# Performance work log

Measured on AMD Instinct MI355X. Metric: run time of the kernel, lower is better.

The kernel has to match this reference:

```python
import jax, jax.numpy as jnp
import numpy as np

N = 100000   # nodes
E = 1600000  # edges (avg degree 16)
D = 128      # in_dim == hidden
L = 3        # num_layers
G = 512      # graphs in batch


def setup_inputs() -> dict:
    key = jax.random.key(0)
    ks = jax.random.split(key, 14)
    s = 0.05
    return {
        "x": jax.random.normal(ks[0], (N, D), jnp.float32),
        "edge_index": jax.random.randint(ks[1], (2, E), 0, N, dtype=jnp.int32),
        "batch": jnp.sort(jax.random.randint(ks[2], (N,), 0, G, dtype=jnp.int32)),
        "W1": jax.random.normal(ks[3], (L, D, D), jnp.float32) * s,
        "b1": jax.random.normal(ks[4], (L, D), jnp.float32) * s,
        "W2": jax.random.normal(ks[5], (L, D, D), jnp.float32) * s,
        "b2": jax.random.normal(ks[6], (L, D), jnp.float32) * s,
        "gamma": jax.random.uniform(ks[7], (L, D), jnp.float32, 0.5, 1.5),
        "beta": jax.random.normal(ks[8], (L, D), jnp.float32) * s,
        "run_mean": jax.random.normal(ks[9], (L, D), jnp.float32) * s,
        "run_var": jax.random.uniform(ks[10], (L, D), jnp.float32, 0.5, 1.5),
        "eps": jnp.zeros((L,), jnp.float32),
        "lin1_W": jax.random.normal(ks[11], (D, D), jnp.float32) * s,
        "lin1_b": jax.random.normal(ks[12], (D,), jnp.float32) * s,
    }


def _bn(h, g, b, m, v):
    # BatchNorm1d in eval mode (running stats)
    return (h - m) * jax.lax.rsqrt(v + 1e-5) * g + b


def reference(x, edge_index, batch, W1, b1, W2, b2, gamma, beta,
              run_mean, run_var, eps, lin1_W, lin1_b):
    n = x.shape[0]
    src, dst = edge_index[0], edge_index[1]
    h = x
    for l in range(L):  # small fixed layer count
        # GINConv: sum-aggregate neighbor features then (1+eps)*self + agg
        agg = jax.ops.segment_sum(h[src], dst, num_segments=n)  # [N, D]
        z = (1.0 + eps[l]) * h + agg
        z = jax.nn.relu(z @ W1[l] + b1[l])
        z = jax.nn.relu(z @ W2[l] + b2[l])
        h = _bn(z, gamma[l], beta[l], run_mean[l], run_var[l])
    # global_mean_pool over graph ids
    counts = jax.ops.segment_sum(jnp.ones((n,), h.dtype), batch, num_segments=G)
    pooled = jax.ops.segment_sum(h, batch, num_segments=G)
    pooled = pooled / jnp.maximum(counts, 1.0)[:, None]  # [G, D]
    # lin1 + ReLU (dropout is identity in eval)
    return jax.nn.relu(pooled @ lin1_W + lin1_b)
```

## Files before the change

### kernel.cpp

```cpp
#include <hip/hip_runtime.h>
#include <hip/hip_bf16.h>

#define NN 100000
#define NE 1600000
#define DD 128
#define NL 3
#define NG 512
#define NBLK ((NN + 255) / 256)
#define CSRP (NE + 8 * NN)
#define NBUCK ((NN + 63) / 64)
#define BSHIFT 9
#define NBUCK2 ((NN + 511) / 512)
#define ABLKS 512
#define ECHUNK (NE / ABLKS)

#define CONV_BLKS 12501
#define PREPW_BLKS 384
#define DEG_BLKS  391
#define INIT_BLKS (CONV_BLKS + PREPW_BLKS + DEG_BLKS)

typedef __attribute__((ext_vector_type(8))) short bf16x8;
typedef __attribute__((ext_vector_type(4))) float f32x4;

__device__ __forceinline__ unsigned short f2bf(float f) {
    union { float f; unsigned int u; } x; x.f = f;
    unsigned int r = x.u + 0x7FFFu + ((x.u >> 16) & 1u);
    return (unsigned short)(r >> 16);
}
__device__ __forceinline__ float bf2f(unsigned short u) {
    union { unsigned int u; float f; } x; x.u = ((unsigned int)u) << 16;
    return x.f;
}
__device__ __forceinline__ float bflo(unsigned int v) { return bf2f((unsigned short)(v & 0xffffu)); }
__device__ __forceinline__ float bfhi(unsigned int v) { return bf2f((unsigned short)(v >> 16)); }
__device__ __forceinline__ unsigned cvtpk(float lo, float hi) {
    unsigned r;
    asm("v_cvt_pk_bf16_f32 %0, %1, %2" : "=v"(r) : "v"(lo), "v"(hi));
    return r;
}

__global__ __launch_bounds__(256) void init_all(const float* __restrict__ x,
                                                unsigned short* __restrict__ h0,
                                                unsigned short* __restrict__ h1,
                                                const float* __restrict__ W1,
                                                const float* __restrict__ W2,
                                                unsigned short* __restrict__ wbf,
                                                int* __restrict__ deg) {
    int bb = blockIdx.x;
    if (bb < CONV_BLKS) {
        long long t = (long long)bb * 256 + threadIdx.x;
        long long base = t * 4;
        if (base < (long long)NN * DD) {
            float4 v = *reinterpret_cast<const float4*>(x + base);
            ushort4 p;
            p.x = f2bf(v.x); p.y = f2bf(v.y); p.z = f2bf(v.z); p.w = f2bf(v.w);
            *reinterpret_cast<ushort4*>(h0 + base) = p;
        } else if (base < (long long)(NN + 1) * DD) {
            ushort4 z = {0, 0, 0, 0};
            *reinterpret_cast<ushort4*>(h0 + base) = z;
            *reinterpret_cast<ushort4*>(h1 + base) = z;
        }
        return;
    }
    bb -= CONV_BLKS;
    if (bb < PREPW_BLKS) {
        int idx = bb * 256 + threadIdx.x;
        int k = idx & 127;
        int n = (idx >> 7) & 127;
        int w = (idx >> 14) & 1;
        int l = idx >> 15;
        const float* src = w ? W2 : W1;
        wbf[idx] = f2bf(src[(l * DD + k) * DD + n]);
        return;
    }
    bb -= PREPW_BLKS;
    int i = bb * 256 + threadIdx.x;
    if (i < NN) deg[i] = 0;
}

__global__ __launch_bounds__(256) void hist_deg(const int* __restrict__ ei,
                                                int* __restrict__ deg) {
    unsigned int e = blockIdx.x * 256u + threadIdx.x;
    atomicAdd(&deg[ei[NE + e]], 1);
}

__global__ __launch_bounds__(256) void scan1(const int* __restrict__ deg,
                                             int* __restrict__ rp,
                                             int* __restrict__ part,
                                             int* __restrict__ bhist) {
    __shared__ int s[256];
    int tid = threadIdx.x;
    int i = blockIdx.x * 256 + tid;
    int vr = (i < NN) ? deg[i] : 0;
    int v = (vr + 7) & ~7;
    s[tid] = v;
    __syncthreads();
    for (int o = 1; o < 256; o <<= 1) {
        int t = (tid >= o) ? s[tid - o] : 0;
        __syncthreads();
        s[tid] += t;
        __syncthreads();
    }
    if (i < NN) rp[i] = s[tid] - v;
    if (tid == 255) part[blockIdx.x] = s[255];
    int bs = vr;
    #pragma unroll
    for (int o = 1; o < 64; o <<= 1) bs += __shfl_xor(bs, o);
    int bucket = blockIdx.x * 4 + (tid >> 6);
    if ((tid & 63) == 0 && bucket < NBUCK) bhist[bucket] = bs;
}

__global__ __launch_bounds__(256) void scan23(int* __restrict__ rp,
                                              const int* __restrict__ part,
                                              const int* __restrict__ deg,
                                              int* __restrict__ csr) {
    __shared__ int red[256];
    int tid = threadIdx.x;
    int bid = blockIdx.x;
    int s = 0;
    for (int i = tid; i < bid; i += 256) s += part[i];
    red[tid] = s;
    __syncthreads();
    for (int o = 128; o > 0; o >>= 1) {
        if (tid < o) red[tid] += red[tid + o];
        __syncthreads();
    }
    int base = red[0];
    int i = bid * 256 + tid;
    if (i < NN) {
        int val = rp[i] + base;
        rp[i] = val;
        int d = deg[i];
        int pd = (d + 7) & ~7;
        for (int j = val + d; j < val + pd; ++j) csr[j] = NN;
        if (i == NN - 1) rp[NN] = val + pd;
    }
}

__global__ __launch_bounds__(256) void bscan(const int* __restrict__ bhist,
                                             int* __restrict__ cboff,
                                             int* __restrict__ gpos) {
    __shared__ int s[256];
    int tid = threadIdx.x;
    int sum = 0;
    if (tid < NBUCK2) {
        #pragma unroll
        for (int j = 0; j < 8; ++j) {
            int f = tid * 8 + j;
            if (f < NBUCK) sum += bhist[f];
        }
    }
    s[tid] = sum;
    __syncthreads();
    for (int o = 1; o < 256; o <<= 1) {
        int t = (tid >= o) ? s[tid - o] : 0;
        __syncthreads();
        s[tid] += t;
        __syncthreads();
    }
    if (tid < NBUCK2) {
        cboff[tid] = s[tid] - sum;
        gpos[tid] = 0;
    }
    if (tid == 0) cboff[NBUCK2] = NE;
}

__global__ __launch_bounds__(256) void binA(const int* __restrict__ ei,
                                            const int* __restrict__ cboff,
                                            int* __restrict__ gpos,
                                            int* __restrict__ ebuf) {
    __shared__ int hist[NBUCK2];
    __shared__ int sbase[NBUCK2];
    int tid = threadIdx.x;
    int e0 = blockIdx.x * ECHUNK;
    for (int i = tid; i < NBUCK2; i += 256) hist[i] = 0;
    __syncthreads();
    for (int i = tid; i < ECHUNK; i += 256) {
        int d = ei[NE + e0 + i];
        atomicAdd(&hist[d >> BSHIFT], 1);
    }
    __syncthreads();
    for (int i = tid; i < NBUCK2; i += 256) {
        int h = hist[i];
        sbase[i] = (h > 0) ? atomicAdd(&gpos[i], h) : 0;
        hist[i] = 0;
    }
    __syncthreads();
    for (int i = tid; i < ECHUNK; i += 256) {
        int s2 = ei[e0 + i];
        int d = ei[NE + e0 + i];
        int b = d >> BSHIFT;
        int pos = atomicAdd(&hist[b], 1);
        ebuf[cboff[b] + sbase[b] + pos] = s2 | ((d & 511) << 17);
    }
}

__global__ __launch_bounds__(256) void binB(const int* __restrict__ ebuf,
                                            const int* __restrict__ cboff,
                                            const int* __restrict__ rp,
                                            int* __restrict__ csr) {
    __shared__ int lcnt[512];
    __shared__ int rpl[512];
    int b = blockIdx.x;
    int tid = threadIdx.x;
    int nb = b << BSHIFT;
    for (int i = tid; i < 512; i += 256) {
        int node = nb + i;
        rpl[i] = (node < NN) ? rp[node] : 0;
        lcnt[i] = 0;
    }
    __syncthreads();
    int st = cboff[b], en = cboff[b + 1];
    for (int i = st + tid; i < en; i += 256) {
        int v = ebuf[i];
        int s2 = v & 0x1FFFF;
        int dl = v >> 17;
        int pos = atomicAdd(&lcnt[dl], 1);
        csr[rpl[dl] + pos] = s2;
    }
}

__global__ __launch_bounds__(256) void layer_fused(
    const unsigned short* __restrict__ hin,
    const int* __restrict__ rp,
    const int* __restrict__ csr,
    const unsigned short* __restrict__ w1t,
    const unsigned short* __restrict__ w2t,
    const float* __restrict__ b1,
    const float* __restrict__ b2,
    const float* __restrict__ gamma,
    const float* __restrict__ beta,
    const float* __restrict__ rmean,
    const float* __restrict__ rvar,
    const float* __restrict__ epsv,
    unsigned short* __restrict__ hout)
{
    __shared__ unsigned short z_lds[16 * 136];
    const int tid = threadIdx.x;
    const int lane = tid & 63;
    const int wave = tid >> 6;
    const int gid = lane >> 4;
    const int lg = lane & 15;
    const int row0 = blockIdx.x * 16;
    const float epl = 1.0f + epsv[0];
    const size_t lgo = (size_t)lg * 8;

#define ACC8(v) do { \
    acc[0] += bflo((v).x); acc[1] += bfhi((v).x); \
    acc[2] += bflo((v).y); acc[3] += bfhi((v).y); \
    acc[4] += bflo((v).z); acc[5] += bfhi((v).z); \
    acc[6] += bflo((v).w); acc[7] += bfhi((v).w); } while (0)

    const int rbase = row0 + (wave << 2);
    int pv = (lane < 5) ? rp[rbase + lane] : 0;
    const int st = __shfl(pv, gid);
    const int en = __shfl(pv, gid + 1);
    const int myrow = rbase + gid;

    float acc[8];
    {
        uint4 sv = *reinterpret_cast<const uint4*>(hin + (size_t)myrow * DD + lgo);
        acc[0] = epl * bflo(sv.x); acc[1] = epl * bfhi(sv.x);
        acc[2] = epl * bflo(sv.y); acc[3] = epl * bfhi(sv.y);
        acc[4] = epl * bflo(sv.z); acc[5] = epl * bfhi(sv.z);
        acc[6] = epl * bflo(sv.w); acc[7] = epl * bfhi(sv.w);
    }
    for (int c0 = st; c0 < en; c0 += 8) {
        int4 idA = *reinterpret_cast<const int4*>(csr + c0);
        int4 idB = *reinterpret_cast<const int4*>(csr + c0 + 4);
        uint4 v0 = *reinterpret_cast<const uint4*>(hin + (size_t)idA.x * DD + lgo);
        uint4 v1 = *reinterpret_cast<const uint4*>(hin + (size_t)idA.y * DD + lgo);
        uint4 v2 = *reinterpret_cast<const uint4*>(hin + (size_t)idA.z * DD + lgo);
        uint4 v3 = *reinterpret_cast<const uint4*>(hin + (size_t)idA.w * DD + lgo);
        uint4 v4 = *reinterpret_cast<const uint4*>(hin + (size_t)idB.x * DD + lgo);
        uint4 v5 = *reinterpret_cast<const uint4*>(hin + (size_t)idB.y * DD + lgo);
        uint4 v6 = *reinterpret_cast<const uint4*>(hin + (size_t)idB.z * DD + lgo);
        uint4 v7 = *reinterpret_cast<const uint4*>(hin + (size_t)idB.w * DD + lgo);
        ACC8(v0); ACC8(v1); ACC8(v2); ACC8(v3);
        ACC8(v4); ACC8(v5); ACC8(v6); ACC8(v7);
    }
    {
        uint4 pk;
        pk.x = cvtpk(acc[0], acc[1]);
        pk.y = cvtpk(acc[2], acc[3]);
        pk.z = cvtpk(acc[4], acc[5]);
        pk.w = cvtpk(acc[6], acc[7]);
        *reinterpret_cast<uint4*>(&z_lds[((wave << 2) + gid) * 136 + lg * 8]) = pk;
    }
    __syncthreads();

    const int l15 = lane & 15;
    const int kq = lane >> 4;
    const int colbase = wave << 5;

    bf16x8 afr[4];
    #pragma unroll
    for (int kk = 0; kk < 4; ++kk)
        afr[kk] = *reinterpret_cast<const bf16x8*>(&z_lds[l15 * 136 + kk * 32 + kq * 8]);
    __syncthreads();

    f32x4 acc4[2];
    #pragma unroll
    for (int nt = 0; nt < 2; ++nt) acc4[nt] = (f32x4){0.f, 0.f, 0.f, 0.f};
    #pragma unroll
    for (int nt = 0; nt < 2; ++nt) {
        #pragma unroll
        for (int kk = 0; kk < 4; ++kk) {
            bf16x8 bfr = *reinterpret_cast<const bf16x8*>(
                w1t + (colbase + nt * 16 + l15) * DD + kk * 32 + kq * 8);
            acc4[nt] = __builtin_amdgcn_mfma_f32_16x16x32_bf16(afr[kk], bfr, acc4[nt], 0, 0, 0);
        }
    }

    #pragma unroll
    for (int nt = 0; nt < 2; ++nt) {
        int col = colbase + nt * 16 + l15;
        float bv = b1[col];
        #pragma unroll
        for (int r = 0; r < 4; ++r) {
            int zr = kq * 4 + r;
            float v = acc4[nt][r] + bv;
            v = v > 0.f ? v : 0.f;
            z_lds[zr * 136 + col] = f2bf(v);
        }
    }
    __syncthreads();

    #pragma unroll
    for (int kk = 0; kk < 4; ++kk)
        afr[kk] = *reinterpret_cast<const bf16x8*>(&z_lds[l15 * 136 + kk * 32 + kq * 8]);
    #pragma unroll
    for (int nt = 0; nt < 2; ++nt) acc4[nt] = (f32x4){0.f, 0.f, 0.f, 0.f};
    #pragma unroll
    for (int nt = 0; nt < 2; ++nt) {
        #pragma unroll
        for (int kk = 0; kk < 4; ++kk) {
            bf16x8 bfr = *reinterpret_cast<const bf16x8*>(
                w2t + (colbase + nt * 16 + l15) * DD + kk * 32 + kq * 8);
            acc4[nt] = __builtin_amdgcn_mfma_f32_16x16x32_bf16(afr[kk], bfr, acc4[nt], 0, 0, 0);
        }
    }

    #pragma unroll
    for (int nt = 0; nt < 2; ++nt) {
        int col = colbase + nt * 16 + l15;
        float bv = b2[col];
        float ga = gamma[col];
        float be = beta[col];
        float mu = rmean[col];
        float inv = rsqrtf(rvar[col] + 1e-5f);
        #pragma unroll
        for (int r = 0; r < 4; ++r) {
            int zr = kq * 4 + r;
            float v = acc4[nt][r] + bv;
            v = v > 0.f ? v : 0.f;
            v = (v - mu) * inv * ga + be;
            hout[(size_t)(row0 + zr) * DD + col] = f2bf(v);
        }
    }
#undef ACC8
}

__global__ __launch_bounds__(256) void pool_final(const unsigned short* __restrict__ h,
                                                  const int* __restrict__ batch,
                                                  const float* __restrict__ W,
                                                  const float* __restrict__ b,
                                                  float* __restrict__ out) {
    int g = blockIdx.x;
    int t = threadIdx.x;
    int c2 = t & 63;
    int qu = t >> 6;

    int lo = 0, hi = NN;
    while (lo < hi) { int mid = (lo + hi) >> 1; if (batch[mid] < g) lo = mid + 1; else hi = mid; }
    int start = lo;
    hi = NN;
    while (lo < hi) { int mid = (lo + hi) >> 1; if (batch[mid] < g + 1) lo = mid + 1; else hi = mid; }
    int end = lo;

    float ax = 0.f, ay = 0.f;
    for (int i = start + qu; i < end; i += 4) {
        unsigned u = *reinterpret_cast<const unsigned*>(h + (size_t)i * DD + c2 * 2);
        ax += bflo(u); ay += bfhi(u);
    }

    __shared__ float ps[4][DD];
    ps[qu][c2 * 2] = ax;
    ps[qu][c2 * 2 + 1] = ay;
    __syncthreads();
    if (t < DD) {
        float inv = 1.0f / fmaxf((float)(end - start), 1.0f);
        ps[0][t] = (ps[0][t] + ps[1][t] + ps[2][t] + ps[3][t]) * inv;
    }
    __syncthreads();
    if (t < DD) {
        float o = b[t];
        #pragma unroll 8
        for (int k = 0; k < DD; ++k)
            o += ps[0][k] * W[k * DD + t];
        out[(size_t)g * DD + t] = fmaxf(o, 0.f);
    }
}

extern "C" void kernel_launch(void* const* d_in, const int* in_sizes, int n_in,
                              void* d_out, int out_size, void* d_ws, size_t ws_size,
                              hipStream_t stream) {
    const float* x     = (const float*)d_in[0];
    const int*   ei    = (const int*)d_in[1];
    const int*   batch = (const int*)d_in[2];
    const float* W1    = (const float*)d_in[3];
    const float* b1    = (const float*)d_in[4];
    const float* W2    = (const float*)d_in[5];
    const float* b2    = (const float*)d_in[6];
    const float* gamma = (const float*)d_in[7];
    const float* beta  = (const float*)d_in[8];
    const float* rmean = (const float*)d_in[9];
    const float* rvar  = (const float*)d_in[10];
    const float* eps   = (const float*)d_in[11];
    const float* lin1W = (const float*)d_in[12];
    const float* lin1b = (const float*)d_in[13];
    float* out = (float*)d_out;

    char* ws = (char*)d_ws;
    size_t off = 0;
    auto alloc = [&](size_t bytes) {
        void* p = ws + off;
        off = (off + bytes + 255) & ~(size_t)255;
        return p;
    };
    unsigned short* h0  = (unsigned short*)alloc((size_t)(NN + 1) * DD * 2);
    unsigned short* h1  = (unsigned short*)alloc((size_t)(NN + 1) * DD * 2);
    int* rp    = (int*)alloc((size_t)(NN + 1) * 4);
    int* deg   = (int*)alloc((size_t)NN * 4);
    int* part  = (int*)alloc(512 * 4);
    int* bhist = (int*)alloc((size_t)NBUCK * 4);
    int* cboff = (int*)alloc((size_t)(NBUCK2 + 1) * 4);
    int* gpos  = (int*)alloc((size_t)NBUCK2 * 4);
    int* csr   = (int*)alloc((size_t)CSRP * 4);
    int* ebuf  = (int*)alloc((size_t)NE * 4);
    unsigned short* wbf = (unsigned short*)alloc((size_t)NL * 2 * DD * DD * 2);

    init_all<<<INIT_BLKS, 256, 0, stream>>>(x, h0, h1, W1, W2, wbf, deg);

    hist_deg<<<NE / 256, 256, 0, stream>>>(ei, deg);
    scan1<<<NBLK, 256, 0, stream>>>(deg, rp, part, bhist);
    scan23<<<NBLK, 256, 0, stream>>>(rp, part, deg, csr);
    bscan<<<1, 256, 0, stream>>>(bhist, cboff, gpos);
    binA<<<ABLKS, 256, 0, stream>>>(ei, cboff, gpos, ebuf);
    binB<<<NBUCK2, 256, 0, stream>>>(ebuf, cboff, rp, csr);

    const int lgrid = NN / 16;
    layer_fused<<<lgrid, 256, 0, stream>>>(
        h0, rp, csr, wbf + 0 * DD * DD, wbf + 1 * DD * DD,
        b1 + 0 * DD, b2 + 0 * DD, gamma + 0 * DD, beta + 0 * DD,
        rmean + 0 * DD, rvar + 0 * DD, eps + 0, h1);
    layer_fused<<<lgrid, 256, 0, stream>>>(
        h1, rp, csr, wbf + 2 * DD * DD, wbf + 3 * DD * DD,
        b1 + 1 * DD, b2 + 1 * DD, gamma + 1 * DD, beta + 1 * DD,
        rmean + 1 * DD, rvar + 1 * DD, eps + 1, h0);
    layer_fused<<<lgrid, 256, 0, stream>>>(
        h0, rp, csr, wbf + 4 * DD * DD, wbf + 5 * DD * DD,
        b1 + 2 * DD, b2 + 2 * DD, gamma + 2 * DD, beta + 2 * DD,
        rmean + 2 * DD, rvar + 2 * DD, eps + 2, h1);

    pool_final<<<NG, 256, 0, stream>>>(h1, batch, lin1W, lin1b, out);
}
```

Before: 519.2 us.

## Build CSR via bucket-local histograms instead of global degree atomics

Replaces the global per-node degree atomic histogram and multi-kernel scan with a per-block shared-memory bucket count, then computes per-node degrees and row pointers locally inside each 512-node bucket after binning. Padding fill moves into the final scatter kernel. The intent is to cut 1.6M global atomics and the scan passes. It also unrolls the neighbor gather loop to 16 edges per iteration for more loads in flight. The trade-off is an extra pass over ebuf and additional small kernel launches.

```diff
diff --git a/kernel.cpp b/kernel.cpp
--- a/kernel.cpp
+++ b/kernel.cpp
@@ -6,9 +6,7 @@
 #define DD 128
 #define NL 3
 #define NG 512
-#define NBLK ((NN + 255) / 256)
 #define CSRP (NE + 8 * NN)
-#define NBUCK ((NN + 63) / 64)
 #define BSHIFT 9
 #define NBUCK2 ((NN + 511) / 512)
 #define ABLKS 512
@@ -16,8 +14,7 @@
 
 #define CONV_BLKS 12501
 #define PREPW_BLKS 384
-#define DEG_BLKS  391
-#define INIT_BLKS (CONV_BLKS + PREPW_BLKS + DEG_BLKS)
+#define INIT_BLKS (CONV_BLKS + PREPW_BLKS + 1)
 
 typedef __attribute__((ext_vector_type(8))) short bf16x8;
 typedef __attribute__((ext_vector_type(4))) float f32x4;
@@ -45,7 +42,7 @@
                                                 const float* __restrict__ W1,
                                                 const float* __restrict__ W2,
                                                 unsigned short* __restrict__ wbf,
-                                                int* __restrict__ deg) {
+                                                int* __restrict__ bcnt) {
     int bb = blockIdx.x;
     if (bb < CONV_BLKS) {
         long long t = (long long)bb * 256 + threadIdx.x;
@@ -73,83 +70,32 @@
         wbf[idx] = f2bf(src[(l * DD + k) * DD + n]);
         return;
     }
-    bb -= PREPW_BLKS;
-    int i = bb * 256 + threadIdx.x;
-    if (i < NN) deg[i] = 0;
-}
-
-__global__ __launch_bounds__(256) void hist_deg(const int* __restrict__ ei,
-                                                int* __restrict__ deg) {
-    unsigned int e = blockIdx.x * 256u + threadIdx.x;
-    atomicAdd(&deg[ei[NE + e]], 1);
-}
-
-__global__ __launch_bounds__(256) void scan1(const int* __restrict__ deg,
-                                             int* __restrict__ rp,
-                                             int* __restrict__ part,
-                                             int* __restrict__ bhist) {
-    __shared__ int s[256];
+    int i = threadIdx.x;
+    if (i < NBUCK2) bcnt[i] = 0;
+}
+
+__global__ __launch_bounds__(256) void bcount(const int* __restrict__ ei,
+                                              int* __restrict__ bcnt) {
+    __shared__ int hist[NBUCK2];
     int tid = threadIdx.x;
-    int i = blockIdx.x * 256 + tid;
-    int vr = (i < NN) ? deg[i] : 0;
-    int v = (vr + 7) & ~7;
-    s[tid] = v;
-    __syncthreads();
-    for (int o = 1; o < 256; o <<= 1) {
-        int t = (tid >= o) ? s[tid - o] : 0;
-        __syncthreads();
-        s[tid] += t;
-        __syncthreads();
-    }
-    if (i < NN) rp[i] = s[tid] - v;
-    if (tid == 255) part[blockIdx.x] = s[255];
-    int bs = vr;
-    #pragma unroll
-    for (int o = 1; o < 64; o <<= 1) bs += __shfl_xor(bs, o);
-    int bucket = blockIdx.x * 4 + (tid >> 6);
-    if ((tid & 63) == 0 && bucket < NBUCK) bhist[bucket] = bs;
-}
-
-__global__ __launch_bounds__(256) void scan23(int* __restrict__ rp,
-                                              const int* __restrict__ part,
-                                              const int* __restrict__ deg,
-                                              int* __restrict__ csr) {
-    __shared__ int red[256];
-    int tid = threadIdx.x;
-    int bid = blockIdx.x;
-    int s = 0;
-    for (int i = tid; i < bid; i += 256) s += part[i];
-    red[tid] = s;
-    __syncthreads();
-    for (int o = 128; o > 0; o >>= 1) {
-        if (tid < o) red[tid] += red[tid + o];
-        __syncthreads();
-    }
-    int base = red[0];
-    int i = bid * 256 + tid;
-    if (i < NN) {
-        int val = rp[i] + base;
-        rp[i] = val;
-        int d = deg[i];
-        int pd = (d + 7) & ~7;
-        for (int j = val + d; j < val + pd; ++j) csr[j] = NN;
-        if (i == NN - 1) rp[NN] = val + pd;
-    }
-}
-
-__global__ __launch_bounds__(256) void bscan(const int* __restrict__ bhist,
+    int e0 = blockIdx.x * ECHUNK;
+    for (int i = tid; i < NBUCK2; i += 256) hist[i] = 0;
+    __syncthreads();
+    for (int i = tid; i < ECHUNK; i += 256)
+        atomicAdd(&hist[ei[NE + e0 + i] >> BSHIFT], 1);
+    __syncthreads();
+    for (int i = tid; i < NBUCK2; i += 256) {
+        int h = hist[i];
+        if (h) atomicAdd(&bcnt[i], h);
+    }
+}
+
+__global__ __launch_bounds__(256) void bscan(const int* __restrict__ bcnt,
                                              int* __restrict__ cboff,
                                              int* __restrict__ gpos) {
     __shared__ int s[256];
     int tid = threadIdx.x;
-    int sum = 0;
-    if (tid < NBUCK2) {
-        #pragma unroll
-        for (int j = 0; j < 8; ++j) {
-            int f = tid * 8 + j;
-            if (f < NBUCK) sum += bhist[f];
-        }
-    }
+    int sum = (tid < NBUCK2) ? bcnt[tid] : 0;
     s[tid] = sum;
     __syncthreads();
     for (int o = 1; o < 256; o <<= 1) {
@@ -195,28 +141,93 @@
     }
 }
 
-__global__ __launch_bounds__(256) void binB(const int* __restrict__ ebuf,
+__global__ __launch_bounds__(256) void bpre(const int* __restrict__ ebuf,
                                             const int* __restrict__ cboff,
-                                            const int* __restrict__ rp,
-                                            int* __restrict__ csr) {
+                                            int* __restrict__ rp,
+                                            int* __restrict__ bsum) {
     __shared__ int lcnt[512];
-    __shared__ int rpl[512];
+    __shared__ int s[256];
     int b = blockIdx.x;
     int tid = threadIdx.x;
-    int nb = b << BSHIFT;
+    lcnt[tid] = 0;
+    lcnt[tid + 256] = 0;
+    __syncthreads();
+    int st = cboff[b], en = cboff[b + 1];
+    for (int i = st + tid; i < en; i += 256)
+        atomicAdd(&lcnt[ebuf[i] >> 17], 1);
+    __syncthreads();
+    int d0 = (lcnt[2 * tid] + 7) & ~7;
+    int d1 = (lcnt[2 * tid + 1] + 7) & ~7;
+    int ps = d0 + d1;
+    s[tid] = ps;
+    __syncthreads();
+    for (int o = 1; o < 256; o <<= 1) {
+        int t = (tid >= o) ? s[tid - o] : 0;
+        __syncthreads();
+        s[tid] += t;
+        __syncthreads();
+    }
+    int base = s[tid] - ps;
+    int node0 = (b << BSHIFT) + 2 * tid;
+    if (node0 < NN) rp[node0] = base;
+    if (node0 + 1 < NN) rp[node0 + 1] = base + d0;
+    if (tid == 255) bsum[b] = s[255];
+}
+
+__global__ __launch_bounds__(256) void bscan2(const int* __restrict__ bsum,
+                                              int* __restrict__ bbase,
+                                              int* __restrict__ rp) {
+    __shared__ int s[256];
+    int tid = threadIdx.x;
+    int sum = (tid < NBUCK2) ? bsum[tid] : 0;
+    s[tid] = sum;
+    __syncthreads();
+    for (int o = 1; o < 256; o <<= 1) {
+        int t = (tid >= o) ? s[tid - o] : 0;
+        __syncthreads();
+        s[tid] += t;
+        __syncthreads();
+    }
+    if (tid < NBUCK2) bbase[tid] = s[tid] - sum;
+    if (tid == 255) rp[NN] = s[255];
+}
+
+__global__ __launch_bounds__(256) void binB2(const int* __restrict__ ebuf,
+                                             const int* __restrict__ cboff,
+                                             const int* __restrict__ bbase,
+                                             int* __restrict__ rp,
+                                             int* __restrict__ csr) {
+    __shared__ int rpl[512];
+    __shared__ int lcnt[512];
+    int b = blockIdx.x;
+    int tid = threadIdx.x;
+    int bb = bbase[b];
     for (int i = tid; i < 512; i += 256) {
-        int node = nb + i;
-        rpl[i] = (node < NN) ? rp[node] : 0;
+        int node = (b << BSHIFT) + i;
+        int v = 0;
+        if (node < NN) {
+            v = rp[node] + bb;
+            rp[node] = v;
+        }
+        rpl[i] = v;
         lcnt[i] = 0;
     }
     __syncthreads();
     int st = cboff[b], en = cboff[b + 1];
     for (int i = st + tid; i < en; i += 256) {
         int v = ebuf[i];
-        int s2 = v & 0x1FFFF;
         int dl = v >> 17;
         int pos = atomicAdd(&lcnt[dl], 1);
-        csr[rpl[dl] + pos] = s2;
+        csr[rpl[dl] + pos] = v & 0x1FFFF;
+    }
+    __syncthreads();
+    for (int i = tid; i < 512; i += 256) {
+        int node = (b << BSHIFT) + i;
+        if (node >= NN) continue;
+        int d = lcnt[i];
+        int pd = (d + 7) & ~7;
+        int base = rpl[i];
+        for (int j = d; j < pd; ++j) csr[base + j] = NN;
     }
 }
 
@@ -265,7 +276,34 @@
         acc[4] = epl * bflo(sv.z); acc[5] = epl * bfhi(sv.z);
         acc[6] = epl * bflo(sv.w); acc[7] = epl * bfhi(sv.w);
     }
-    for (int c0 = st; c0 < en; c0 += 8) {
+    int c0 = st;
+    for (; c0 + 16 <= en; c0 += 16) {
+        int4 idA = *reinterpret_cast<const int4*>(csr + c0);
+        int4 idB = *reinterpret_cast<const int4*>(csr + c0 + 4);
+        int4 idC = *reinterpret_cast<const int4*>(csr + c0 + 8);
+        int4 idD = *reinterpret_cast<const int4*>(csr + c0 + 12);
+        uint4 v0 = *reinterpret_cast<const uint4*>(hin + (size_t)idA.x * DD + lgo);
+        uint4 v1 = *reinterpret_cast<const uint4*>(hin + (size_t)idA.y * DD + lgo);
+        uint4 v2 = *reinterpret_cast<const uint4*>(hin + (size_t)idA.z * DD + lgo);
+        uint4 v3 = *reinterpret_cast<const uint4*>(hin + (size_t)idA.w * DD + lgo);
+        uint4 v4 = *reinterpret_cast<const uint4*>(hin + (size_t)idB.x * DD + lgo);
+        uint4 v5 = *reinterpret_cast<const uint4*>(hin + (size_t)idB.y * DD + lgo);
+        uint4 v6 = *reinterpret_cast<const uint4*>(hin + (size_t)idB.z * DD + lgo);
+        uint4 v7 = *reinterpret_cast<const uint4*>(hin + (size_t)idB.w * DD + lgo);
+        uint4 v8 = *reinterpret_cast<const uint4*>(hin + (size_t)idC.x * DD + lgo);
+        uint4 v9 = *reinterpret_cast<const uint4*>(hin + (size_t)idC.y * DD + lgo);
+        uint4 va = *reinterpret_cast<const uint4*>(hin + (size_t)idC.z * DD + lgo);
+        uint4 vb = *reinterpret_cast<const uint4*>(hin + (size_t)idC.w * DD + lgo);
+        uint4 vc = *reinterpret_cast<const uint4*>(hin + (size_t)idD.x * DD + lgo);
+        uint4 vd = *reinterpret_cast<const uint4*>(hin + (size_t)idD.y * DD + lgo);
+        uint4 ve = *reinterpret_cast<const uint4*>(hin + (size_t)idD.z * DD + lgo);
+        uint4 vf = *reinterpret_cast<const uint4*>(hin + (size_t)idD.w * DD + lgo);
+        ACC8(v0); ACC8(v1); ACC8(v2); ACC8(v3);
+        ACC8(v4); ACC8(v5); ACC8(v6); ACC8(v7);
+        ACC8(v8); ACC8(v9); ACC8(va); ACC8(vb);
+        ACC8(vc); ACC8(vd); ACC8(ve); ACC8(vf);
+    }
+    if (c0 < en) {
         int4 idA = *reinterpret_cast<const int4*>(csr + c0);
         int4 idB = *reinterpret_cast<const int4*>(csr + c0 + 4);
         uint4 v0 = *reinterpret_cast<const uint4*>(hin + (size_t)idA.x * DD + lgo);
@@ -431,23 +469,23 @@
     unsigned short* h0  = (unsigned short*)alloc((size_t)(NN + 1) * DD * 2);
     unsigned short* h1  = (unsigned short*)alloc((size_t)(NN + 1) * DD * 2);
     int* rp    = (int*)alloc((size_t)(NN + 1) * 4);
-    int* deg   = (int*)alloc((size_t)NN * 4);
-    int* part  = (int*)alloc(512 * 4);
-    int* bhist = (int*)alloc((size_t)NBUCK * 4);
+    int* bcnt  = (int*)alloc((size_t)NBUCK2 * 4);
     int* cboff = (int*)alloc((size_t)(NBUCK2 + 1) * 4);
     int* gpos  = (int*)alloc((size_t)NBUCK2 * 4);
+    int* bsum  = (int*)alloc((size_t)NBUCK2 * 4);
+    int* bbase = (int*)alloc((size_t)NBUCK2 * 4);
     int* csr   = (int*)alloc((size_t)CSRP * 4);
     int* ebuf  = (int*)alloc((size_t)NE * 4);
     unsigned short* wbf = (unsigned short*)alloc((size_t)NL * 2 * DD * DD * 2);
 
-    init_all<<<INIT_BLKS, 256, 0, stream>>>(x, h0, h1, W1, W2, wbf, deg);
-
-    hist_deg<<<NE / 256, 256, 0, stream>>>(ei, deg);
-    scan1<<<NBLK, 256, 0, stream>>>(deg, rp, part, bhist);
-    scan23<<<NBLK, 256, 0, stream>>>(rp, part, deg, csr);
-    bscan<<<1, 256, 0, stream>>>(bhist, cboff, gpos);
+    init_all<<<INIT_BLKS, 256, 0, stream>>>(x, h0, h1, W1, W2, wbf, bcnt);
+
+    bcount<<<ABLKS, 256, 0, stream>>>(ei, bcnt);
+    bscan<<<1, 256, 0, stream>>>(bcnt, cboff, gpos);
     binA<<<ABLKS, 256, 0, stream>>>(ei, cboff, gpos, ebuf);
-    binB<<<NBUCK2, 256, 0, stream>>>(ebuf, cboff, rp, csr);
+    bpre<<<NBUCK2, 256, 0, stream>>>(ebuf, cboff, rp, bsum);
+    bscan2<<<1, 256, 0, stream>>>(bsum, bbase, rp);
+    binB2<<<NBUCK2, 256, 0, stream>>>(ebuf, cboff, bbase, rp, csr);
 
     const int lgrid = NN / 16;
     layer_fused<<<lgrid, 256, 0, stream>>>(
```

Result: faster. 473.5 us (-8.8%).
